# Kernel tuning notes

Measured on AMD Instinct MI355X. Metric: run time of the kernel, lower is better.

Reference implementation:

```python
import jax, jax.numpy as jnp
import numpy as np
from jax import lax

B, TENC, TMEL = 32, 512, 400
E, H, A, P, M, F, K = 512, 512, 512, 256, 128, 32, 31


def setup_inputs() -> dict:
    key = jax.random.key(0)
    ks = jax.random.split(key, 20)
    def rn(i, shape, fan_in):
        return jax.random.normal(ks[i], shape, jnp.float32) / np.float32(np.sqrt(fan_in))
    return dict(
        enc_outputs=jax.random.normal(ks[0], (B, TENC, 2 * E), jnp.float32),
        mel_spec_true=jax.random.normal(ks[1], (B, TMEL, M), jnp.float32),
        text_lens=jax.random.randint(ks[2], (B,), 0, TENC),
        mel_spec_lens=jax.random.randint(ks[3], (B,), 0, TMEL),
        max_text_len=TENC,
        pre_w1=rn(4, (M, P), M), pre_w2=rn(5, (P, P), P),
        attn_wi=rn(6, (P + E, 3 * H), P + E), attn_wh=rn(7, (H, 3 * H), H),
        attn_bi=jnp.zeros((3 * H,), jnp.float32), attn_bh=jnp.zeros((3 * H,), jnp.float32),
        q_w=rn(8, (H, A), H), k_w=rn(9, (2 * E, A), 2 * E),
        score_w=rn(10, (A, 1), A), score_b=jnp.zeros((1,), jnp.float32),
        loc_conv_w=rn(11, (F, 2, K), 2 * K), loc_w=rn(12, (F, A), F), loc_b=jnp.zeros((A,), jnp.float32),
        out_wi=rn(13, (A + H, 3 * H), A + H), out_wh=rn(14, (H, 3 * H), H),
        out_bi=jnp.zeros((3 * H,), jnp.float32), out_bh=jnp.zeros((3 * H,), jnp.float32),
        dec_w=rn(15, (H + A, M), H + A), dec_b=jnp.zeros((M,), jnp.float32),
        gate_w=rn(16, (H + A, 1), H + A), gate_b=jnp.zeros((1,), jnp.float32),
    )


def _gru_step(x, h, wi, wh, bi, bh):
    # single-step torch nn.GRU cell; gate order r, z, n
    gi = x @ wi + bi
    gh = h @ wh + bh
    ir, iz, inn = jnp.split(gi, 3, axis=-1)
    hr, hz, hn = jnp.split(gh, 3, axis=-1)
    r = jax.nn.sigmoid(ir + hr)
    z = jax.nn.sigmoid(iz + hz)
    n = jnp.tanh(inn + r * hn)
    return (1.0 - z) * n + z * h


def reference(enc_outputs, mel_spec_true, text_lens, mel_spec_lens, max_text_len,
              pre_w1, pre_w2, attn_wi, attn_wh, attn_bi, attn_bh,
              q_w, k_w, score_w, score_b, loc_conv_w, loc_w, loc_b,
              out_wi, out_wh, out_bi, out_bh, dec_w, dec_b, gate_w, gate_b):
    Bsz, Tenc, _ = enc_outputs.shape
    Tmel = mel_spec_true.shape[1]
    Hd = attn_wh.shape[0]
    Ad = k_w.shape[1]
    pad = (loc_conv_w.shape[2] - 1) // 2

    keys_p = enc_outputs @ k_w                                # [B,Tenc,A]
    enc_mask = jnp.arange(Tenc)[None, :] > text_lens[:, None]  # True = masked (t > len)

    def prenet(x):  # dropout disabled for determinism
        return jax.nn.relu(jax.nn.relu(x @ pre_w1) @ pre_w2)

    dec_in0 = prenet(jnp.zeros((Bsz, mel_spec_true.shape[2]), enc_outputs.dtype))
    carry0 = (jnp.zeros((Bsz, Hd), jnp.float32), jnp.zeros((Bsz, Hd), jnp.float32),
              jnp.zeros((Bsz, Tenc), jnp.float32), jnp.zeros((Bsz, Tenc), jnp.float32),
              jnp.zeros((Bsz, Ad), jnp.float32), dec_in0)

    def step(carry, _):
        h_attn, h_out, att_w, att_cum, ctx, dec_in = carry
        h_attn = _gru_step(jnp.concatenate([dec_in, ctx], -1), h_attn, attn_wi, attn_wh, attn_bi, attn_bh)
        loc_in = jnp.stack([att_w, att_cum], axis=1)           # [B,2,Tenc]
        loc = lax.conv_general_dilated(loc_in, loc_conv_w, (1,), [(pad, pad)],
                                       dimension_numbers=('NCH', 'OIH', 'NCH'))  # [B,F,Tenc]
        loc = jnp.swapaxes(loc, 1, 2) @ loc_w + loc_b          # [B,Tenc,A]
        q = (h_attn @ q_w)[:, None, :]                         # [B,1,A]
        s = (jnp.tanh(q + keys_p + loc) @ score_w + score_b)[..., 0]  # [B,Tenc]
        s = jnp.where(enc_mask, -jnp.inf, s)
        att_w = jax.nn.softmax(s, axis=1)
        ctx = jnp.einsum('bt,bta->ba', att_w, keys_p)
        att_cum = att_cum + att_w
        h_out = _gru_step(jnp.concatenate([h_attn, ctx], -1), h_out, out_wi, out_wh, out_bi, out_bh)
        att_h = jnp.concatenate([h_out, ctx], -1)
        mel = att_h @ dec_w + dec_b                            # [B,M]
        stop = (att_h @ gate_w + gate_b)[:, 0]                 # [B]
        dec_in = prenet(mel)                                   # teacher_force_ratio = 0
        return (h_attn, h_out, att_w, att_cum, ctx, dec_in), (mel, stop, att_w)

    _, (mels, gates, attns) = lax.scan(step, carry0, None, length=Tmel)
    mels = jnp.swapaxes(mels, 0, 1)    # [B,Tmel,M]
    gates = jnp.swapaxes(gates, 0, 1)  # [B,Tmel]
    attns = jnp.swapaxes(attns, 0, 1)  # [B,Tmel,Tenc]
    mel_mask = jnp.arange(Tmel)[None, :] > mel_spec_lens[:, None]
    masked_mel = jnp.where(mel_mask[:, :, None], 0.0, mels)
    masked_gate = jnp.where(mel_mask, 1000.0, gates)
    return masked_mel, masked_gate, attns, mel_mask
```

## Files before the change

kernel.cpp:

```cpp
#include <hip/hip_runtime.h>
#include <hip/hip_fp16.h>
#include <math.h>

#define NBLK 256
#define NTHR 1024

__device__ __forceinline__ float fast_rcp(float x) {
#if __has_builtin(__builtin_amdgcn_rcpf)
  return __builtin_amdgcn_rcpf(x);
#else
  return 1.f / x;
#endif
}
__device__ __forceinline__ float fast_sigmoid(float x) { return fast_rcp(1.f + __expf(-x)); }
__device__ __forceinline__ float fast_tanh(float x) { return 1.f - 2.f * fast_rcp(1.f + __expf(2.f * x)); }

union HU2 { unsigned int u; __half2 h; };
union HU4 { uint4 u; __half2 h[4]; };
__device__ __forceinline__ float2 cvt2(unsigned int u) { HU2 t; t.u = u; return __half22float2(t.h); }

__device__ __forceinline__ void sta(float* p, float v) {
  __hip_atomic_store(p, v, __ATOMIC_RELAXED, __HIP_MEMORY_SCOPE_AGENT);
}
__device__ __forceinline__ float lda(const float* p) {
  return __hip_atomic_load(p, __ATOMIC_RELAXED, __HIP_MEMORY_SCOPE_AGENT);
}
__device__ __forceinline__ int ldai(const int* p) {
  return __hip_atomic_load(p, __ATOMIC_RELAXED, __HIP_MEMORY_SCOPE_AGENT);
}
__device__ __forceinline__ void ntst(float* p, float v) { __builtin_nontemporal_store(v, p); }

struct Params {
  const float *enc, *pre_w1, *pre_w2, *attn_bi, *attn_bh;
  const float *q_w, *k_w, *score_w, *score_b, *conv_w, *loc_w, *loc_b;
  const float *out_bi, *out_bh, *dec_b, *gate_b;
  const float *attn_wi, *attn_wh, *out_wi, *out_wh, *dec_w, *gate_w;
  const int *text_lens, *mel_lens;
  __half *hkeys, *gw1T, *gw2T, *decT, *pre1T, *pre2T, *gateh, *locwh, *qwT;
  float *hA, *hO, *attw, *attcum, *decin, *ebuf, *zpart, *ctxacc, *ctxacc2, *stateZ;
  float *qbuf;
  int *done, *zdone, *done2, *hAdone, *qdone;
  float *out_mel, *out_gate, *out_attn, *out_mask;
};

__global__ __launch_bounds__(512) void k_keys(Params p) {
  __shared__ float sA[16][132];
  __shared__ float sB[16][68];
  int tid = threadIdx.x;
  int row0 = blockIdx.x * 128, col0 = blockIdx.y * 64;
  float acc[4][4] = {};
  int r = tid >> 2, kq = tid & 3;
  int tx = tid & 15, ty = tid >> 4;
  for (int k0 = 0; k0 < 1024; k0 += 16) {
    __syncthreads();
    float4 a4 = *(const float4*)(p.enc + (size_t)(row0 + r) * 1024 + k0 + kq * 4);
    sA[kq * 4 + 0][r] = a4.x; sA[kq * 4 + 1][r] = a4.y;
    sA[kq * 4 + 2][r] = a4.z; sA[kq * 4 + 3][r] = a4.w;
    if (tid < 256) {
      int kb = tid >> 4, nb = (tid & 15) * 4;
      float4 b4 = *(const float4*)(p.k_w + (size_t)(k0 + kb) * 512 + col0 + nb);
      sB[kb][nb + 0] = b4.x; sB[kb][nb + 1] = b4.y;
      sB[kb][nb + 2] = b4.z; sB[kb][nb + 3] = b4.w;
    }
    __syncthreads();
#pragma unroll
    for (int k = 0; k < 16; k++) {
      float ar[4], br[4];
#pragma unroll
      for (int i = 0; i < 4; i++) { ar[i] = sA[k][ty * 4 + i]; br[i] = sB[k][tx * 4 + i]; }
#pragma unroll
      for (int i = 0; i < 4; i++)
#pragma unroll
        for (int j = 0; j < 4; j++) acc[i][j] = fmaf(ar[i], br[j], acc[i][j]);
    }
  }
#pragma unroll
  for (int i = 0; i < 4; i++)
#pragma unroll
    for (int j = 0; j < 4; j++)
      p.hkeys[(size_t)(row0 + ty * 4 + i) * 512 + col0 + tx * 4 + j] = __float2half(acc[i][j]);
}

__global__ __launch_bounds__(256) void k_repack(Params p) {
  const int gsz = gridDim.x * 256;
  const int t0 = blockIdx.x * 256 + threadIdx.x;
  for (int i = t0; i < 1280 * 512; i += gsz) {
    int r = i >> 9, u = i & 511;
    const float* src = (r < 768) ? p.attn_wi + (size_t)r * 1536 : p.attn_wh + (size_t)(r - 768) * 1536;
    __half2* d = (__half2*)(p.gw1T + ((size_t)i << 2));
    d[0] = __halves2half2(__float2half(src[u]), __float2half(src[512 + u]));
    d[1] = __halves2half2(__float2half(src[1024 + u]), __float2half(0.f));
  }
  for (int i = t0; i < 1536 * 512; i += gsz) {
    int r = i >> 9, u = i & 511;
    const float* src = (r < 1024) ? p.out_wi + (size_t)r * 1536 : p.out_wh + (size_t)(r - 1024) * 1536;
    __half2* d = (__half2*)(p.gw2T + ((size_t)i << 2));
    d[0] = __halves2half2(__float2half(src[u]), __float2half(src[512 + u]));
    d[1] = __halves2half2(__float2half(src[1024 + u]), __float2half(0.f));
  }
  for (int i = t0; i < 512 * 512; i += gsz) {
    int k = i >> 9, a = i & 511;
    p.qwT[(size_t)a * 512 + k] = __float2half(p.q_w[(size_t)k * 512 + a]);
  }
  for (int i = t0; i < 1024 * 128; i += gsz) {
    int k = i >> 7, m = i & 127;
    p.decT[(size_t)m * 1024 + k] = __float2half(p.dec_w[(size_t)k * 128 + m]);
  }
  for (int i = t0; i < 1024; i += gsz) p.gateh[i] = __float2half(p.gate_w[i]);
  for (int i = t0; i < 16384; i += gsz) p.locwh[i] = __float2half(p.loc_w[i]);
  for (int i = t0; i < 128 * 256; i += gsz) {
    int m = i >> 8, pc = i & 255;
    p.pre1T[(size_t)pc * 128 + m] = __float2half(p.pre_w1[(size_t)m * 256 + pc]);
  }
  for (int i = t0; i < 256 * 256; i += gsz) {
    int k = i >> 8, pc = i & 255;
    p.pre2T[(size_t)pc * 256 + k] = __float2half(p.pre_w2[(size_t)k * 256 + pc]);
  }
  for (int i = t0; i < 106496; i += gsz) p.stateZ[i] = 0.f;
  for (int i = t0; i < 16384; i += gsz) p.ctxacc[i] = 0.f;
  for (int i = t0; i < 16384; i += gsz) p.ctxacc2[i] = 0.f;
  for (int i = t0; i < 512; i += gsz) p.qdone[i] = 0;
  for (int i = t0; i < 2048; i += gsz) p.zdone[i] = 0;
  for (int i = t0; i < 12800; i += gsz) {
    int b = i / 400, t = i - b * 400;
    p.out_mask[i] = (t > p.mel_lens[b]) ? 1.f : 0.f;
  }
}

struct SMemMega {
  __half keysL[64 * 512];
  float ctxL[4][520];
  float hA2[4][520];
  float hO2[4][520];
  float invZ[4];
  union {
    struct { float x[4][264]; float4 part4[16][64]; } gr;
    struct { float locS[64][33]; float aw[94]; float ac[94]; float hA_s[512];
             float qS[512]; float qp2[16][64]; float cpred[8][512]; float eS[64]; } s3;
    struct { float xh[1024]; float red[1024]; float mel[128]; float p1[256]; } s6;
  } u;
};

__device__ __forceinline__ void gchunk(const uint2* __restrict__ w,
                                       const float* __restrict__ x, int ks,
                                       int j0, int j1,
                                       float& a0, float& a1, float& a2) {
#pragma unroll 8
  for (int j = j0; j < j1; ++j) {
    uint2 wv = w[(size_t)j << 13];
    float xv = x[ks + (j << 4)];
    float2 f0 = cvt2(wv.x);
    float nf = cvt2(wv.y).x;
    a0 = fmaf(xv, f0.x, a0);
    a1 = fmaf(xv, f0.y, a1);
    a2 = fmaf(xv, nf, a2);
  }
}

__global__ __launch_bounds__(NTHR) void mega(Params p) {
  __shared__ SMemMega sm;
  const int blk = blockIdx.x, tid = threadIdx.x;
  const int ug = blk & 31, bg = blk >> 5, b0 = bg * 4;
  const int bS = blk & 31, t8 = blk >> 5, t0g = t8 << 6;

  const int u_ = tid & 15, b2_ = (tid >> 4) & 3, ks_ = tid >> 6;
  const int uG_ = (ug << 4) + u_;
  const uint2* w1 = (const uint2*)p.gw1T + ((size_t)ks_ << 9) + uG_;
  const uint2* w2 = (const uint2*)p.gw2T + ((size_t)ks_ << 9) + uG_;

  {
    const uint4* src = (const uint4*)(p.hkeys + (((size_t)(bS << 9) + t0g) << 9));
    uint4* dst = (uint4*)sm.keysL;
    for (int i = tid; i < 4096; i += NTHR) dst[i] = src[i];
    for (int i = tid; i < 2048; i += NTHR) sm.ctxL[i >> 9][i & 511] = 0.f;
  }
  __syncthreads();

  float g1r = 0.f, g1z = 0.f, g1ni = 0.f, g1nh = 0.f;

#pragma clang loop unroll(disable)
  for (int step = 0; step < 400; step++) {
    const int par = step & 1;
    float* hA_prev = p.hA + par * 16384;
    float* hA_next = p.hA + (par ^ 1) * 16384;
    float* hO_prev = p.hO + par * 16384;
    float* hO_next = p.hO + (par ^ 1) * 16384;
    float* cCur = par ? p.ctxacc2 : p.ctxacc;
    float* cNxt = par ? p.ctxacc : p.ctxacc2;

    float r2 = 0.f, z2 = 0.f, ni2 = 0.f, nh2 = 0.f;

    {
      if (step > 0) {
        if (tid < 4) {
          while (ldai(&p.done2[(b0 + tid) * 16]) < 4 * step)
            __builtin_amdgcn_s_sleep(2);
        }
        __syncthreads();
      }
      for (int i = tid; i < 1024; i += NTHR)
        sm.u.gr.x[i >> 8][i & 255] = lda(&p.decin[((b0 + (i >> 8)) << 8) + (i & 255)]);
      for (int i = tid; i < 2048; i += NTHR)
        sm.hO2[i >> 9][i & 511] = lda(&hO_prev[((b0 + (i >> 9)) << 9) + (i & 511)]);
      __syncthreads();
      gchunk(w1, &sm.u.gr.x[b2_][0], ks_, 0, 16, g1r, g1z, g1ni);
      sm.u.gr.part4[ks_][(u_ << 2) + b2_] = make_float4(g1r, g1z, g1ni, g1nh);
      __syncthreads();
      if (tid < 64) {
        int uu = tid >> 2, bb2 = tid & 3;
        float4 s = make_float4(0.f, 0.f, 0.f, 0.f);
#pragma unroll
        for (int l = 0; l < 16; l++) {
          float4 v = sm.u.gr.part4[l][(uu << 2) + bb2];
          s.x += v.x; s.y += v.y; s.z += v.z; s.w += v.w;
        }
        int uGf = (ug << 4) + uu;
        float r = fast_sigmoid(s.x + p.attn_bi[uGf] + p.attn_bh[uGf]);
        float z = fast_sigmoid(s.y + p.attn_bi[512 + uGf] + p.attn_bh[512 + uGf]);
        float n = fast_tanh(s.z + p.attn_bi[1024 + uGf] + r * (s.w + p.attn_bh[1024 + uGf]));
        float hv = lda(&hA_prev[((b0 + bb2) << 9) + uGf]);
        sta(&hA_next[((b0 + bb2) << 9) + uGf], (1.f - z) * n + z * hv);
      }
      asm volatile("s_waitcnt vmcnt(0)" ::: "memory");
      if (tid < 4) atomicAdd(&p.hAdone[(b0 + tid) * 16], 1);
      gchunk(w2, &sm.hO2[b2_][0] - 1024, ks_, 64, 96, r2, z2, nh2);
    }

    {
      for (int j = tid; j < 94; j += NTHR) {
        int pp = t0g - 15 + j;
        bool ok = (unsigned)pp < 512u;
        sm.u.s3.aw[j] = ok ? lda(&p.attw[(bS << 9) + pp]) : 0.f;
        sm.u.s3.ac[j] = ok ? lda(&p.attcum[(bS << 9) + pp]) : 0.f;
      }
      if (tid == 0) {
        while (ldai(&p.hAdone[bS * 16]) < 32 * (step + 1))
          __builtin_amdgcn_s_sleep(2);
      }
      __syncthreads();
      if (t8 == 0) {
        for (int i = tid; i < 512; i += NTHR) sta(&cNxt[(bS << 9) + i], 0.f);
      }
      if (tid < 512) sm.u.s3.hA_s[tid] = lda(&hA_next[(bS << 9) + tid]);
      __syncthreads();
      {
        int a = tid & 63, ks = tid >> 6;
        const HU4* qp = (const HU4*)(p.qwT + (size_t)(t0g + a) * 512 + ks * 32);
        float q0 = 0.f, q1 = 0.f;
#pragma unroll
        for (int it = 0; it < 4; it++) {
          HU4 raw = qp[it];
          int kb = ks * 32 + it * 8;
#pragma unroll
          for (int h2 = 0; h2 < 4; h2++) {
            float2 w = __half22float2(raw.h[h2]);
            q0 = fmaf(sm.u.s3.hA_s[kb + h2 * 2], w.x, q0);
            q1 = fmaf(sm.u.s3.hA_s[kb + h2 * 2 + 1], w.y, q1);
          }
        }
        sm.u.s3.qp2[ks][a] = q0 + q1;
      }
      __syncthreads();
      if (tid < 64) {
        float s = 0.f;
#pragma unroll
        for (int l = 0; l < 16; l++) s += sm.u.s3.qp2[l][tid];
        sta(&p.qbuf[(bS << 9) + t0g + tid], s + p.loc_b[t0g + tid]);
      }
      if (tid == 0) {
        asm volatile("s_waitcnt vmcnt(0)" ::: "memory");
        atomicAdd(&p.qdone[bS * 16], 1);
      }
      const int tlen = p.text_lens[bS];
      for (int i = tid; i < 2048; i += NTHR) {
        int tt = i >> 5, f = i & 31;
        const float* w0 = p.conv_w + f * 62;
        float a = 0.f;
#pragma unroll
        for (int k = 0; k < 31; k++)
          a = fmaf(w0[k], sm.u.s3.aw[tt + k], fmaf(w0[31 + k], sm.u.s3.ac[tt + k], a));
        sm.u.s3.locS[tt][f] = a;
      }
      if (tid == 0) {
        while (ldai(&p.qdone[bS * 16]) < 8 * (step + 1))
          __builtin_amdgcn_s_sleep(2);
      }
      __syncthreads();
      if (tid < 512) sm.u.s3.qS[tid] = lda(&p.qbuf[(bS << 9) + tid]);
      __syncthreads();
      const int lane = tid & 63, wv = tid >> 6;
      float acc[4][8];
      float4 qA = *(const float4*)&sm.u.s3.qS[lane * 8];
      float4 qB = *(const float4*)&sm.u.s3.qS[lane * 8 + 4];
#pragma unroll
      for (int j = 0; j < 4; j++) {
        int tL = wv * 4 + j;
        HU4 raw; raw.u = *(const uint4*)&sm.keysL[tL * 512 + lane * 8];
        float2 k0 = __half22float2(raw.h[0]), k1 = __half22float2(raw.h[1]);
        float2 k2 = __half22float2(raw.h[2]), k3 = __half22float2(raw.h[3]);
        acc[j][0] = qA.x + k0.x; acc[j][1] = qA.y + k0.y;
        acc[j][2] = qA.z + k1.x; acc[j][3] = qA.w + k1.y;
        acc[j][4] = qB.x + k2.x; acc[j][5] = qB.y + k2.y;
        acc[j][6] = qB.z + k3.x; acc[j][7] = qB.w + k3.y;
      }
#pragma unroll 4
      for (int f = 0; f < 32; f++) {
        HU4 rw; rw.u = *(const uint4*)(p.locwh + (size_t)f * 512 + lane * 8);
        float2 w0 = __half22float2(rw.h[0]), w1 = __half22float2(rw.h[1]);
        float2 w2v = __half22float2(rw.h[2]), w3 = __half22float2(rw.h[3]);
#pragma unroll
        for (int j = 0; j < 4; j++) {
          float lf = sm.u.s3.locS[wv * 4 + j][f];
          acc[j][0] = fmaf(lf, w0.x, acc[j][0]); acc[j][1] = fmaf(lf, w0.y, acc[j][1]);
          acc[j][2] = fmaf(lf, w1.x, acc[j][2]); acc[j][3] = fmaf(lf, w1.y, acc[j][3]);
          acc[j][4] = fmaf(lf, w2v.x, acc[j][4]); acc[j][5] = fmaf(lf, w2v.y, acc[j][5]);
          acc[j][6] = fmaf(lf, w3.x, acc[j][6]); acc[j][7] = fmaf(lf, w3.y, acc[j][7]);
        }
      }
      float4 sA = *(const float4*)(p.score_w + lane * 8);
      float4 sB = *(const float4*)(p.score_w + lane * 8 + 4);
      float sbias = p.score_b[0];
      float e_reg[4];
#pragma unroll
      for (int j = 0; j < 4; j++) {
        float pv = fast_tanh(acc[j][0]) * sA.x + fast_tanh(acc[j][1]) * sA.y +
                   fast_tanh(acc[j][2]) * sA.z + fast_tanh(acc[j][3]) * sA.w +
                   fast_tanh(acc[j][4]) * sB.x + fast_tanh(acc[j][5]) * sB.y +
                   fast_tanh(acc[j][6]) * sB.z + fast_tanh(acc[j][7]) * sB.w;
#pragma unroll
        for (int off = 32; off > 0; off >>= 1) pv += __shfl_xor(pv, off, 64);
        int t = t0g + wv * 4 + j;
        e_reg[j] = (t > tlen) ? 0.f : __expf(pv + sbias);
      }
      if (lane == 0) {
#pragma unroll
        for (int j = 0; j < 4; j++) sm.u.s3.eS[wv * 4 + j] = e_reg[j];
      }
      float cp[8] = {0.f, 0.f, 0.f, 0.f, 0.f, 0.f, 0.f, 0.f};
#pragma unroll
      for (int j = 0; j < 4; j++) {
        int tL = wv * 4 + j;
        HU4 raw; raw.u = *(const uint4*)&sm.keysL[tL * 512 + lane * 8];
        float2 k0 = __half22float2(raw.h[0]), k1 = __half22float2(raw.h[1]);
        float2 k2 = __half22float2(raw.h[2]), k3 = __half22float2(raw.h[3]);
        float e = e_reg[j];
        cp[0] = fmaf(e, k0.x, cp[0]); cp[1] = fmaf(e, k0.y, cp[1]);
        cp[2] = fmaf(e, k1.x, cp[2]); cp[3] = fmaf(e, k1.y, cp[3]);
        cp[4] = fmaf(e, k2.x, cp[4]); cp[5] = fmaf(e, k2.y, cp[5]);
        cp[6] = fmaf(e, k3.x, cp[6]); cp[7] = fmaf(e, k3.y, cp[7]);
      }
      __syncthreads();
      if (wv < 8) {
        float4* r0 = (float4*)&sm.u.s3.cpred[wv][lane * 8];
        r0[0] = make_float4(cp[0], cp[1], cp[2], cp[3]);
        r0[1] = make_float4(cp[4], cp[5], cp[6], cp[7]);
      }
      __syncthreads();
      if (wv >= 8) {
        float* r0 = &sm.u.s3.cpred[wv - 8][lane * 8];
#pragma unroll
        for (int i = 0; i < 8; i++) r0[i] += cp[i];
      }
      __syncthreads();
      if (tid < 512) {
        float s = 0.f;
#pragma unroll
        for (int j = 0; j < 8; j++) s += sm.u.s3.cpred[j][tid];
        atomicAdd(&cCur[(bS << 9) + tid], s);
      }
      if (tid < 64) {
        float e = sm.u.s3.eS[tid];
        sta(&p.ebuf[(bS << 9) + t0g + tid], e);
        float z = e;
#pragma unroll
        for (int off = 32; off > 0; off >>= 1) z += __shfl_xor(z, off, 64);
        if (tid == 0) sta(&p.zpart[bS * 8 + t8], z);
      }
      if (tid < 512 && (tid & 63) == 0) {
        asm volatile("s_waitcnt vmcnt(0)" ::: "memory");
        atomicAdd(&p.zdone[bS * 16], 1);
      }
      if (tid < 4) {
        while (ldai(&p.hAdone[(b0 + tid) * 16]) < 32 * (step + 1))
          __builtin_amdgcn_s_sleep(2);
      }
      __syncthreads();
      for (int i = tid; i < 2048; i += NTHR)
        sm.hA2[i >> 9][i & 511] = lda(&hA_next[((b0 + (i >> 9)) << 9) + (i & 511)]);
      __syncthreads();
      gchunk(w2, &sm.hA2[b2_][0], ks_, 0, 32, r2, z2, ni2);
    }

    {
      if (tid < 4) {
        while (ldai(&p.zdone[(b0 + tid) * 16]) < 64 * (step + 1))
          __builtin_amdgcn_s_sleep(2);
        float Z = 0.f;
#pragma unroll
        for (int j = 0; j < 8; j++) Z += lda(&p.zpart[(b0 + tid) * 8 + j]);
        sm.invZ[tid] = fast_rcp(Z);
      }
      __syncthreads();
      for (int i = tid; i < 2048; i += NTHR) {
        int b2 = i >> 9, a = i & 511;
        sm.ctxL[b2][a] = lda(&cCur[((b0 + b2) << 9) + a]) * sm.invZ[b2];
      }
      if (ug < 4) {
        const int bb = b0 + ug;
        if (tid < 512) {
          float v = lda(&p.ebuf[(bb << 9) + tid]) * sm.invZ[ug];
          sta(&p.attw[(bb << 9) + tid], v);
          float oc = lda(&p.attcum[(bb << 9) + tid]);
          sta(&p.attcum[(bb << 9) + tid], oc + v);
          ntst(&p.out_attn[(size_t)bb * 204800 + (size_t)step * 512 + tid], v);
        }
      }
      __syncthreads();
      gchunk(w2, &sm.ctxL[b2_][0] - 512, ks_, 32, 64, r2, z2, ni2);
      sm.u.gr.part4[ks_][(u_ << 2) + b2_] = make_float4(r2, z2, ni2, nh2);
      __syncthreads();
      if (tid < 64) {
        int uu = tid >> 2, bb2 = tid & 3;
        float4 s = make_float4(0.f, 0.f, 0.f, 0.f);
#pragma unroll
        for (int l = 0; l < 16; l++) {
          float4 v = sm.u.gr.part4[l][(uu << 2) + bb2];
          s.x += v.x; s.y += v.y; s.z += v.z; s.w += v.w;
        }
        int uGf = (ug << 4) + uu;
        float r = fast_sigmoid(s.x + p.out_bi[uGf] + p.out_bh[uGf]);
        float z = fast_sigmoid(s.y + p.out_bi[512 + uGf] + p.out_bh[512 + uGf]);
        float n = fast_tanh(s.z + p.out_bi[1024 + uGf] + r * (s.w + p.out_bh[1024 + uGf]));
        float hv = sm.hO2[bb2][uGf];
        sta(&hO_next[((b0 + bb2) << 9) + uGf], (1.f - z) * n + z * hv);
      }
      asm volatile("s_waitcnt vmcnt(0)" ::: "memory");
      if (tid < 4) atomicAdd(&p.done[(b0 + tid) * 16], 1);
      if (ug < 4) {
        const int bb = b0 + ug;
        if (tid == 0) {
          int target = 32 * (step + 1);
          while (ldai(&p.done[bb * 16]) < target)
            __builtin_amdgcn_s_sleep(2);
        }
        __syncthreads();
        sm.u.s6.xh[tid] = (tid < 512) ? lda(&hO_next[(bb << 9) + tid])
                                      : sm.ctxL[ug][tid - 512];
        __syncthreads();
        bool masked = step > p.mel_lens[bb];
        {
          int m = tid & 127, ks = tid >> 7;
          const HU4* dp = (const HU4*)(p.decT + (size_t)m * 1024 + ks * 128);
          float a = 0.f;
#pragma unroll 4
          for (int it = 0; it < 16; it++) {
            HU4 raw = dp[it];
            int kb = ks * 128 + it * 8;
#pragma unroll
            for (int h2 = 0; h2 < 4; h2++) {
              float2 w = __half22float2(raw.h[h2]);
              a = fmaf(sm.u.s6.xh[kb + h2 * 2], w.x, a);
              a = fmaf(sm.u.s6.xh[kb + h2 * 2 + 1], w.y, a);
            }
          }
          sm.u.s6.red[tid] = a;
        }
        __syncthreads();
        if (tid < 128) {
          float mv = p.dec_b[tid];
#pragma unroll
          for (int j = 0; j < 8; j++) mv += sm.u.s6.red[tid + j * 128];
          sm.u.s6.mel[tid] = mv;
          ntst(&p.out_mel[(size_t)bb * 51200 + (size_t)step * 128 + tid], masked ? 0.f : mv);
        }
        __syncthreads();
        sm.u.s6.red[tid] = sm.u.s6.xh[tid] * __half2float(p.gateh[tid]);
        __syncthreads();
        if (tid < 64) {
          float g = 0.f;
#pragma unroll
          for (int j = 0; j < 16; j++) g += sm.u.s6.red[tid + j * 64];
#pragma unroll
          for (int off = 32; off > 0; off >>= 1) g += __shfl_xor(g, off, 64);
          if (tid == 0) ntst(&p.out_gate[bb * 400 + step], masked ? 1000.f : (g + p.gate_b[0]));
        }
        __syncthreads();
        {
          int pc = tid & 255, ks = tid >> 8;
          const HU4* wp = (const HU4*)(p.pre1T + (size_t)pc * 128 + ks * 32);
          float a = 0.f;
#pragma unroll
          for (int it = 0; it < 4; it++) {
            HU4 raw = wp[it];
            int kb = ks * 32 + it * 8;
#pragma unroll
            for (int h2 = 0; h2 < 4; h2++) {
              float2 w = __half22float2(raw.h[h2]);
              a = fmaf(sm.u.s6.mel[kb + h2 * 2], w.x, a);
              a = fmaf(sm.u.s6.mel[kb + h2 * 2 + 1], w.y, a);
            }
          }
          sm.u.s6.red[tid] = a;
        }
        __syncthreads();
        if (tid < 256) {
          float a = sm.u.s6.red[tid] + sm.u.s6.red[tid + 256] +
                    sm.u.s6.red[tid + 512] + sm.u.s6.red[tid + 768];
          sm.u.s6.p1[tid] = fmaxf(a, 0.f);
        }
        __syncthreads();
        {
          int pc = tid & 255, ks = tid >> 8;
          const HU4* wp = (const HU4*)(p.pre2T + (size_t)pc * 256 + ks * 64);
          float a = 0.f;
#pragma unroll
          for (int it = 0; it < 8; it++) {
            HU4 raw = wp[it];
            int kb = ks * 64 + it * 8;
#pragma unroll
            for (int h2 = 0; h2 < 4; h2++) {
              float2 w = __half22float2(raw.h[h2]);
              a = fmaf(sm.u.s6.p1[kb + h2 * 2], w.x, a);
              a = fmaf(sm.u.s6.p1[kb + h2 * 2 + 1], w.y, a);
            }
          }
          sm.u.s6.red[tid] = a;
        }
        __syncthreads();
        if (tid < 256) {
          float a = sm.u.s6.red[tid] + sm.u.s6.red[tid + 256] +
                    sm.u.s6.red[tid + 512] + sm.u.s6.red[tid + 768];
          sta(&p.decin[(bb << 8) + tid], fmaxf(a, 0.f));
        }
        if (tid < 256 && (tid & 63) == 0) {
          asm volatile("s_waitcnt vmcnt(0)" ::: "memory");
          atomicAdd(&p.done2[bb * 16], 1);
        }
      }
      g1r = 0.f; g1z = 0.f; g1ni = 0.f; g1nh = 0.f;
      if (step < 399) {
        gchunk(w1, &sm.ctxL[b2_][0] - 256, ks_, 16, 48, g1r, g1z, g1ni);
        gchunk(w1, &sm.hA2[b2_][0] - 768, ks_, 48, 80, g1r, g1z, g1nh);
      }
    }
  }
}

extern "C" void kernel_launch(void* const* d_in, const int* in_sizes, int n_in,
                              void* d_out, int out_size, void* d_ws, size_t ws_size,
                              hipStream_t stream) {
  Params p;
  p.enc       = (const float*)d_in[0];
  p.text_lens = (const int*)d_in[2];
  p.mel_lens  = (const int*)d_in[3];
  p.pre_w1    = (const float*)d_in[5];
  p.pre_w2    = (const float*)d_in[6];
  p.attn_wi   = (const float*)d_in[7];
  p.attn_wh   = (const float*)d_in[8];
  p.attn_bi   = (const float*)d_in[9];
  p.attn_bh   = (const float*)d_in[10];
  p.q_w       = (const float*)d_in[11];
  p.k_w       = (const float*)d_in[12];
  p.score_w   = (const float*)d_in[13];
  p.score_b   = (const float*)d_in[14];
  p.conv_w    = (const float*)d_in[15];
  p.loc_w     = (const float*)d_in[16];
  p.loc_b     = (const float*)d_in[17];
  p.out_wi    = (const float*)d_in[18];
  p.out_wh    = (const float*)d_in[19];
  p.out_bi    = (const float*)d_in[20];
  p.out_bh    = (const float*)d_in[21];
  p.dec_w     = (const float*)d_in[22];
  p.dec_b     = (const float*)d_in[23];
  p.gate_w    = (const float*)d_in[24];
  p.gate_b    = (const float*)d_in[25];

  float* ws = (float*)d_ws;
  p.hkeys  = (__half*)(ws);
  p.gw1T   = (__half*)(ws + 4194304);
  p.gw2T   = (__half*)(ws + 5505024);
  p.decT   = (__half*)(ws + 7077888);
  p.pre1T  = (__half*)(ws + 7143424);
  p.pre2T  = (__half*)(ws + 7159808);
  p.gateh  = (__half*)(ws + 7192576);
  p.locwh  = (__half*)(ws + 7193088);
  p.qwT    = (__half*)(ws + 7201280);
  p.hA     = ws + 7332352;
  p.hO     = ws + 7365120;
  p.attw   = ws + 7397888;
  p.attcum = ws + 7414272;
  p.decin  = ws + 7430656;
  p.stateZ = p.hA;
  p.ebuf   = ws + 7438848;
  p.zpart  = ws + 7455232;
  p.ctxacc = ws + 7455488;
  p.qdone  = (int*)(ws + 7471904);
  p.ctxacc2 = ws + 7472416;
  p.zdone  = (int*)(ws + 7488800);
  p.done2  = (int*)(ws + 7489312);
  p.hAdone = (int*)(ws + 7489824);
  p.done   = (int*)(ws + 7490336);
  p.qbuf   = ws + 7490848;
  float* out = (float*)d_out;
  p.out_mel  = out;
  p.out_gate = out + 1638400;
  p.out_attn = out + 1651200;
  p.out_mask = out + 8204800;

  k_repack<<<2048, 256, 0, stream>>>(p);
  k_keys<<<dim3(128, 8), 512, 0, stream>>>(p);
  void* args[] = { (void*)&p };
  hipLaunchCooperativeKernel((const void*)mega, dim3(NBLK), dim3(NTHR), args, 0, stream);
}
```

Before: 37.60 ms.

## Distribute query and mel/gate projections across GRU blocks via partial sums

Each block that updates a 16-unit slice of the attention GRU now also computes a partial query projection from fp32 q_w and writes it to a partial buffer. Each block that updates a slice of the output GRU likewise computes partial mel and gate projections. Consumers then sum these partials, which removes the separate qbuf/qdone stage and the serial decoder matvec done by a few blocks. Completion counters now work per batch group with wave-granular increments, and a start-up barrier lets the partial buffers reuse the half-precision key workspace once every block has copied its keys into shared memory. The cost is more partial-sum traffic and fp32 weight reads in place of fp16 repacked weights.

Measured after the change: 53.33 ms. 41.8% more time.

```diff
diff --git a/kernel.cpp b/kernel.cpp
--- a/kernel.cpp
+++ b/kernel.cpp
@@ -36,10 +36,10 @@
   const float *out_bi, *out_bh, *dec_b, *gate_b;
   const float *attn_wi, *attn_wh, *out_wi, *out_wh, *dec_w, *gate_w;
   const int *text_lens, *mel_lens;
-  __half *hkeys, *gw1T, *gw2T, *decT, *pre1T, *pre2T, *gateh, *locwh, *qwT;
+  __half *hkeys, *gw1T, *gw2T, *pre1T, *pre2T, *locwh;
   float *hA, *hO, *attw, *attcum, *decin, *ebuf, *zpart, *ctxacc, *ctxacc2, *stateZ;
-  float *qbuf;
-  int *done, *zdone, *done2, *hAdone, *qdone;
+  float *qpart, *melpart, *gatepart;
+  int *done, *zdone, *done2, *hAdone, *initbar;
   float *out_mel, *out_gate, *out_attn, *out_mask;
 };
 
@@ -98,15 +98,6 @@
     d[0] = __halves2half2(__float2half(src[u]), __float2half(src[512 + u]));
     d[1] = __halves2half2(__float2half(src[1024 + u]), __float2half(0.f));
   }
-  for (int i = t0; i < 512 * 512; i += gsz) {
-    int k = i >> 9, a = i & 511;
-    p.qwT[(size_t)a * 512 + k] = __float2half(p.q_w[(size_t)k * 512 + a]);
-  }
-  for (int i = t0; i < 1024 * 128; i += gsz) {
-    int k = i >> 7, m = i & 127;
-    p.decT[(size_t)m * 1024 + k] = __float2half(p.dec_w[(size_t)k * 128 + m]);
-  }
-  for (int i = t0; i < 1024; i += gsz) p.gateh[i] = __float2half(p.gate_w[i]);
   for (int i = t0; i < 16384; i += gsz) p.locwh[i] = __float2half(p.loc_w[i]);
   for (int i = t0; i < 128 * 256; i += gsz) {
     int m = i >> 8, pc = i & 255;
@@ -119,7 +110,6 @@
   for (int i = t0; i < 106496; i += gsz) p.stateZ[i] = 0.f;
   for (int i = t0; i < 16384; i += gsz) p.ctxacc[i] = 0.f;
   for (int i = t0; i < 16384; i += gsz) p.ctxacc2[i] = 0.f;
-  for (int i = t0; i < 512; i += gsz) p.qdone[i] = 0;
   for (int i = t0; i < 2048; i += gsz) p.zdone[i] = 0;
   for (int i = t0; i < 12800; i += gsz) {
     int b = i / 400, t = i - b * 400;
@@ -134,10 +124,11 @@
   float hO2[4][520];
   float invZ[4];
   union {
-    struct { float x[4][264]; float4 part4[16][64]; } gr;
-    struct { float locS[64][33]; float aw[94]; float ac[94]; float hA_s[512];
-             float qS[512]; float qp2[16][64]; float cpred[8][512]; float eS[64]; } s3;
-    struct { float xh[1024]; float red[1024]; float mel[128]; float p1[256]; } s6;
+    struct { float x[4][264]; float4 part4[16][64];
+             float hAslice[4][16]; float hOslice[4][16]; } gr;
+    struct { float locS[64][33]; float aw[94]; float ac[94];
+             float qS[512]; float cpred[8][512]; float eS[64]; } s3;
+    struct { float red[1024]; float mel[132]; float p1[264]; } s6;
   } u;
 };
 
@@ -162,6 +153,7 @@
   const int blk = blockIdx.x, tid = threadIdx.x;
   const int ug = blk & 31, bg = blk >> 5, b0 = bg * 4;
   const int bS = blk & 31, t8 = blk >> 5, t0g = t8 << 6;
+  const int bgS = bS >> 2;
 
   const int u_ = tid & 15, b2_ = (tid >> 4) & 3, ks_ = tid >> 6;
   const int uG_ = (ug << 4) + u_;
@@ -172,7 +164,16 @@
     const uint4* src = (const uint4*)(p.hkeys + (((size_t)(bS << 9) + t0g) << 9));
     uint4* dst = (uint4*)sm.keysL;
     for (int i = tid; i < 4096; i += NTHR) dst[i] = src[i];
-    for (int i = tid; i < 2048; i += NTHR) sm.ctxL[i >> 9][i & 511] = 0.f;
+    for (int i = tid; i < 2048; i += NTHR) {
+      sm.ctxL[i >> 9][i & 511] = 0.f;
+      sm.hA2[i >> 9][i & 511] = 0.f;
+      sm.hO2[i >> 9][i & 511] = 0.f;
+    }
+  }
+  __syncthreads();
+  if (tid == 0) {
+    atomicAdd(p.initbar, 1);
+    while (ldai(p.initbar) < NBLK) __builtin_amdgcn_s_sleep(2);
   }
   __syncthreads();
 
@@ -192,8 +193,8 @@
 
     {
       if (step > 0) {
-        if (tid < 4) {
-          while (ldai(&p.done2[(b0 + tid) * 16]) < 4 * step)
+        if (tid == 0) {
+          while (ldai(&p.done2[bg * 16]) < 16 * step)
             __builtin_amdgcn_s_sleep(2);
         }
         __syncthreads();
@@ -219,58 +220,44 @@
         float z = fast_sigmoid(s.y + p.attn_bi[512 + uGf] + p.attn_bh[512 + uGf]);
         float n = fast_tanh(s.z + p.attn_bi[1024 + uGf] + r * (s.w + p.attn_bh[1024 + uGf]));
         float hv = lda(&hA_prev[((b0 + bb2) << 9) + uGf]);
-        sta(&hA_next[((b0 + bb2) << 9) + uGf], (1.f - z) * n + z * hv);
-      }
-      asm volatile("s_waitcnt vmcnt(0)" ::: "memory");
-      if (tid < 4) atomicAdd(&p.hAdone[(b0 + tid) * 16], 1);
+        float hnew = (1.f - z) * n + z * hv;
+        sta(&hA_next[((b0 + bb2) << 9) + uGf], hnew);
+        sm.u.gr.hAslice[bb2][uu] = hnew;
+      }
+      __syncthreads();
+      {
+        int a = tid & 511, bh = tid >> 9;
+        const float* qw = p.q_w + ((size_t)(ug << 4)) * 512 + a;
+        float s0 = 0.f, s1 = 0.f;
+#pragma unroll
+        for (int u = 0; u < 16; u++) {
+          float w = qw[(size_t)u * 512];
+          s0 = fmaf(sm.u.gr.hAslice[bh * 2][u], w, s0);
+          s1 = fmaf(sm.u.gr.hAslice[bh * 2 + 1][u], w, s1);
+        }
+        int base = ((((b0 + bh * 2) << 5) | ug) << 9) + a;
+        sta(&p.qpart[base], s0);
+        sta(&p.qpart[base + (1 << 14)], s1);
+      }
+      if ((tid & 63) == 0) {
+        asm volatile("s_waitcnt vmcnt(0)" ::: "memory");
+        atomicAdd(&p.hAdone[bg * 16], 1);
+      }
       gchunk(w2, &sm.hO2[b2_][0] - 1024, ks_, 64, 96, r2, z2, nh2);
     }
 
     {
+      __syncthreads();
       for (int j = tid; j < 94; j += NTHR) {
         int pp = t0g - 15 + j;
         bool ok = (unsigned)pp < 512u;
         sm.u.s3.aw[j] = ok ? lda(&p.attw[(bS << 9) + pp]) : 0.f;
         sm.u.s3.ac[j] = ok ? lda(&p.attcum[(bS << 9) + pp]) : 0.f;
       }
-      if (tid == 0) {
-        while (ldai(&p.hAdone[bS * 16]) < 32 * (step + 1))
-          __builtin_amdgcn_s_sleep(2);
-      }
-      __syncthreads();
       if (t8 == 0) {
         for (int i = tid; i < 512; i += NTHR) sta(&cNxt[(bS << 9) + i], 0.f);
       }
-      if (tid < 512) sm.u.s3.hA_s[tid] = lda(&hA_next[(bS << 9) + tid]);
-      __syncthreads();
-      {
-        int a = tid & 63, ks = tid >> 6;
-        const HU4* qp = (const HU4*)(p.qwT + (size_t)(t0g + a) * 512 + ks * 32);
-        float q0 = 0.f, q1 = 0.f;
-#pragma unroll
-        for (int it = 0; it < 4; it++) {
-          HU4 raw = qp[it];
-          int kb = ks * 32 + it * 8;
-#pragma unroll
-          for (int h2 = 0; h2 < 4; h2++) {
-            float2 w = __half22float2(raw.h[h2]);
-            q0 = fmaf(sm.u.s3.hA_s[kb + h2 * 2], w.x, q0);
-            q1 = fmaf(sm.u.s3.hA_s[kb + h2 * 2 + 1], w.y, q1);
-          }
-        }
-        sm.u.s3.qp2[ks][a] = q0 + q1;
-      }
-      __syncthreads();
-      if (tid < 64) {
-        float s = 0.f;
-#pragma unroll
-        for (int l = 0; l < 16; l++) s += sm.u.s3.qp2[l][tid];
-        sta(&p.qbuf[(bS << 9) + t0g + tid], s + p.loc_b[t0g + tid]);
-      }
-      if (tid == 0) {
-        asm volatile("s_waitcnt vmcnt(0)" ::: "memory");
-        atomicAdd(&p.qdone[bS * 16], 1);
-      }
+      __syncthreads();
       const int tlen = p.text_lens[bS];
       for (int i = tid; i < 2048; i += NTHR) {
         int tt = i >> 5, f = i & 31;
@@ -282,11 +269,21 @@
         sm.u.s3.locS[tt][f] = a;
       }
       if (tid == 0) {
-        while (ldai(&p.qdone[bS * 16]) < 8 * (step + 1))
+        while (ldai(&p.hAdone[bgS * 16]) < 512 * (step + 1))
           __builtin_amdgcn_s_sleep(2);
       }
       __syncthreads();
-      if (tid < 512) sm.u.s3.qS[tid] = lda(&p.qbuf[(bS << 9) + tid]);
+      {
+        int a = tid & 511, h = tid >> 9;
+        const float* qp = p.qpart + (((size_t)(bS << 5) + (h << 4)) << 9) + a;
+        float s = 0.f;
+#pragma unroll
+        for (int g = 0; g < 16; g++) s += lda(qp + ((size_t)g << 9));
+        sm.u.s3.cpred[h][a] = s;
+      }
+      __syncthreads();
+      if (tid < 512)
+        sm.u.s3.qS[tid] = sm.u.s3.cpred[0][tid] + sm.u.s3.cpred[1][tid] + p.loc_b[tid];
       __syncthreads();
       const int lane = tid & 63, wv = tid >> 6;
       float acc[4][8];
@@ -378,10 +375,10 @@
       }
       if (tid < 512 && (tid & 63) == 0) {
         asm volatile("s_waitcnt vmcnt(0)" ::: "memory");
-        atomicAdd(&p.zdone[bS * 16], 1);
-      }
-      if (tid < 4) {
-        while (ldai(&p.hAdone[(b0 + tid) * 16]) < 32 * (step + 1))
+        atomicAdd(&p.zdone[bgS * 16], 1);
+      }
+      if (tid == 0) {
+        while (ldai(&p.hAdone[bg * 16]) < 512 * (step + 1))
           __builtin_amdgcn_s_sleep(2);
       }
       __syncthreads();
@@ -392,9 +389,12 @@
     }
 
     {
+      if (tid == 0) {
+        while (ldai(&p.zdone[bg * 16]) < 256 * (step + 1))
+          __builtin_amdgcn_s_sleep(2);
+      }
+      __syncthreads();
       if (tid < 4) {
-        while (ldai(&p.zdone[(b0 + tid) * 16]) < 64 * (step + 1))
-          __builtin_amdgcn_s_sleep(2);
         float Z = 0.f;
 #pragma unroll
         for (int j = 0; j < 8; j++) Z += lda(&p.zpart[(b0 + tid) * 8 + j]);
@@ -405,15 +405,13 @@
         int b2 = i >> 9, a = i & 511;
         sm.ctxL[b2][a] = lda(&cCur[((b0 + b2) << 9) + a]) * sm.invZ[b2];
       }
-      if (ug < 4) {
+      if (ug < 4 && tid < 512) {
         const int bb = b0 + ug;
-        if (tid < 512) {
-          float v = lda(&p.ebuf[(bb << 9) + tid]) * sm.invZ[ug];
-          sta(&p.attw[(bb << 9) + tid], v);
-          float oc = lda(&p.attcum[(bb << 9) + tid]);
-          sta(&p.attcum[(bb << 9) + tid], oc + v);
-          ntst(&p.out_attn[(size_t)bb * 204800 + (size_t)step * 512 + tid], v);
-        }
+        float v = lda(&p.ebuf[(bb << 9) + tid]) * sm.invZ[ug];
+        sta(&p.attw[(bb << 9) + tid], v);
+        float oc = lda(&p.attcum[(bb << 9) + tid]);
+        sta(&p.attcum[(bb << 9) + tid], oc + v);
+        ntst(&p.out_attn[(size_t)bb * 204800 + (size_t)step * 512 + tid], v);
       }
       __syncthreads();
       gchunk(w2, &sm.ctxL[b2_][0] - 512, ks_, 32, 64, r2, z2, ni2);
@@ -432,57 +430,65 @@
         float z = fast_sigmoid(s.y + p.out_bi[512 + uGf] + p.out_bh[512 + uGf]);
         float n = fast_tanh(s.z + p.out_bi[1024 + uGf] + r * (s.w + p.out_bh[1024 + uGf]));
         float hv = sm.hO2[bb2][uGf];
-        sta(&hO_next[((b0 + bb2) << 9) + uGf], (1.f - z) * n + z * hv);
-      }
-      asm volatile("s_waitcnt vmcnt(0)" ::: "memory");
-      if (tid < 4) atomicAdd(&p.done[(b0 + tid) * 16], 1);
+        float hnew = (1.f - z) * n + z * hv;
+        sta(&hO_next[((b0 + bb2) << 9) + uGf], hnew);
+        sm.u.gr.hOslice[bb2][uu] = hnew;
+      }
+      __syncthreads();
+      if (tid < 512) {
+        int b = tid >> 7, m = tid & 127;
+        const float* dw = p.dec_w + ((size_t)(ug << 4)) * 128 + m;
+        const float* dw2 = p.dec_w + ((size_t)(512 + (ug << 4))) * 128 + m;
+        float a = 0.f;
+#pragma unroll
+        for (int u = 0; u < 16; u++) {
+          a = fmaf(sm.u.gr.hOslice[b][u], dw[(size_t)u * 128], a);
+          a = fmaf(sm.ctxL[b][(ug << 4) + u], dw2[(size_t)u * 128], a);
+        }
+        sta(&p.melpart[((((b0 + b) << 5) | ug) << 7) + m], a);
+        if (m == 0) {
+          const float* gw = p.gate_w + (ug << 4);
+          float g = 0.f;
+#pragma unroll
+          for (int u = 0; u < 16; u++) {
+            g = fmaf(sm.u.gr.hOslice[b][u], gw[u], g);
+            g = fmaf(sm.ctxL[b][(ug << 4) + u], gw[512 + u], g);
+          }
+          sta(&p.gatepart[((b0 + b) << 5) | ug], g);
+        }
+      }
+      if ((tid & 63) == 0) {
+        asm volatile("s_waitcnt vmcnt(0)" ::: "memory");
+        atomicAdd(&p.done[bg * 16], 1);
+      }
+      g1r = 0.f; g1z = 0.f; g1ni = 0.f; g1nh = 0.f;
+      if (step < 399) {
+        gchunk(w1, &sm.ctxL[b2_][0] - 256, ks_, 16, 48, g1r, g1z, g1ni);
+        gchunk(w1, &sm.hA2[b2_][0] - 768, ks_, 48, 80, g1r, g1z, g1nh);
+      }
       if (ug < 4) {
         const int bb = b0 + ug;
         if (tid == 0) {
-          int target = 32 * (step + 1);
-          while (ldai(&p.done[bb * 16]) < target)
+          while (ldai(&p.done[bg * 16]) < 512 * (step + 1))
             __builtin_amdgcn_s_sleep(2);
         }
-        __syncthreads();
-        sm.u.s6.xh[tid] = (tid < 512) ? lda(&hO_next[(bb << 9) + tid])
-                                      : sm.ctxL[ug][tid - 512];
         __syncthreads();
         bool masked = step > p.mel_lens[bb];
-        {
-          int m = tid & 127, ks = tid >> 7;
-          const HU4* dp = (const HU4*)(p.decT + (size_t)m * 1024 + ks * 128);
-          float a = 0.f;
-#pragma unroll 4
-          for (int it = 0; it < 16; it++) {
-            HU4 raw = dp[it];
-            int kb = ks * 128 + it * 8;
-#pragma unroll
-            for (int h2 = 0; h2 < 4; h2++) {
-              float2 w = __half22float2(raw.h[h2]);
-              a = fmaf(sm.u.s6.xh[kb + h2 * 2], w.x, a);
-              a = fmaf(sm.u.s6.xh[kb + h2 * 2 + 1], w.y, a);
-            }
-          }
-          sm.u.s6.red[tid] = a;
-        }
-        __syncthreads();
         if (tid < 128) {
+          const float* mp = p.melpart + (((size_t)(bb << 5)) << 7) + tid;
           float mv = p.dec_b[tid];
 #pragma unroll
-          for (int j = 0; j < 8; j++) mv += sm.u.s6.red[tid + j * 128];
+          for (int g = 0; g < 32; g++) mv += lda(mp + (g << 7));
           sm.u.s6.mel[tid] = mv;
           ntst(&p.out_mel[(size_t)bb * 51200 + (size_t)step * 128 + tid], masked ? 0.f : mv);
         }
-        __syncthreads();
-        sm.u.s6.red[tid] = sm.u.s6.xh[tid] * __half2float(p.gateh[tid]);
-        __syncthreads();
-        if (tid < 64) {
-          float g = 0.f;
-#pragma unroll
-          for (int j = 0; j < 16; j++) g += sm.u.s6.red[tid + j * 64];
-#pragma unroll
-          for (int off = 32; off > 0; off >>= 1) g += __shfl_xor(g, off, 64);
-          if (tid == 0) ntst(&p.out_gate[bb * 400 + step], masked ? 1000.f : (g + p.gate_b[0]));
+        if (tid >= 128 && tid < 192) {
+          int l = tid & 63;
+          float g = (l < 32) ? lda(&p.gatepart[(bb << 5) + l]) : 0.f;
+#pragma unroll
+          for (int off = 16; off > 0; off >>= 1) g += __shfl_xor(g, off, 64);
+          if (l == 0)
+            ntst(&p.out_gate[bb * 400 + step], masked ? 1000.f : (g + p.gate_b[0]));
         }
         __syncthreads();
         {
@@ -534,13 +540,8 @@
         }
         if (tid < 256 && (tid & 63) == 0) {
           asm volatile("s_waitcnt vmcnt(0)" ::: "memory");
-          atomicAdd(&p.done2[bb * 16], 1);
-        }
-      }
-      g1r = 0.f; g1z = 0.f; g1ni = 0.f; g1nh = 0.f;
-      if (step < 399) {
-        gchunk(w1, &sm.ctxL[b2_][0] - 256, ks_, 16, 48, g1r, g1z, g1ni);
-        gchunk(w1, &sm.hA2[b2_][0] - 768, ks_, 48, 80, g1r, g1z, g1nh);
+          atomicAdd(&p.done2[bg * 16], 1);
+        }
       }
     }
   }
@@ -577,14 +578,14 @@
 
   float* ws = (float*)d_ws;
   p.hkeys  = (__half*)(ws);
+  p.qpart  = ws;
+  p.melpart = ws + 524288;
+  p.gatepart = ws + 655360;
   p.gw1T   = (__half*)(ws + 4194304);
   p.gw2T   = (__half*)(ws + 5505024);
-  p.decT   = (__half*)(ws + 7077888);
   p.pre1T  = (__half*)(ws + 7143424);
   p.pre2T  = (__half*)(ws + 7159808);
-  p.gateh  = (__half*)(ws + 7192576);
   p.locwh  = (__half*)(ws + 7193088);
-  p.qwT    = (__half*)(ws + 7201280);
   p.hA     = ws + 7332352;
   p.hO     = ws + 7365120;
   p.attw   = ws + 7397888;
@@ -594,13 +595,13 @@
   p.ebuf   = ws + 7438848;
   p.zpart  = ws + 7455232;
   p.ctxacc = ws + 7455488;
-  p.qdone  = (int*)(ws + 7471904);
   p.ctxacc2 = ws + 7472416;
-  p.zdone  = (int*)(ws + 7488800);
-  p.done2  = (int*)(ws + 7489312);
-  p.hAdone = (int*)(ws + 7489824);
-  p.done   = (int*)(ws + 7490336);
-  p.qbuf   = ws + 7490848;
+  int* fb  = (int*)(ws + 7488800);
+  p.zdone  = fb;
+  p.done2  = fb + 128;
+  p.hAdone = fb + 256;
+  p.done   = fb + 384;
+  p.initbar = fb + 1920;
   float* out = (float*)d_out;
   p.out_mel  = out;
   p.out_gate = out + 1638400;
```

## Coarsen sync flags to batch groups and hoist location conv before waits

Applied to the files above, without the earlier changes.

Per-batch completion counters become per-batch-group counters, so one thread polls a single flag instead of four threads polling four. The location convolution and the location-weight projection now run before waiting on the hA and q flags, overlapping that work with the producer latency. The next step's input-GRU partial products are issued right after the hO update, before the decoder wait, instead of at the end of the step. The flag buffers are relaid out into one contiguous region with a new zeroing pass, adding some risk around counter targets and initialization.

New measurement: 37.33 ms. About the same (-0.7%).

```diff
diff --git a/kernel.cpp b/kernel.cpp
--- a/kernel.cpp
+++ b/kernel.cpp
@@ -119,8 +119,7 @@
   for (int i = t0; i < 106496; i += gsz) p.stateZ[i] = 0.f;
   for (int i = t0; i < 16384; i += gsz) p.ctxacc[i] = 0.f;
   for (int i = t0; i < 16384; i += gsz) p.ctxacc2[i] = 0.f;
-  for (int i = t0; i < 512; i += gsz) p.qdone[i] = 0;
-  for (int i = t0; i < 2048; i += gsz) p.zdone[i] = 0;
+  for (int i = t0; i < 2048; i += gsz) p.hAdone[i] = 0;
   for (int i = t0; i < 12800; i += gsz) {
     int b = i / 400, t = i - b * 400;
     p.out_mask[i] = (t > p.mel_lens[b]) ? 1.f : 0.f;
@@ -162,6 +161,7 @@
   const int blk = blockIdx.x, tid = threadIdx.x;
   const int ug = blk & 31, bg = blk >> 5, b0 = bg * 4;
   const int bS = blk & 31, t8 = blk >> 5, t0g = t8 << 6;
+  const int bgS = bS >> 2;
 
   const int u_ = tid & 15, b2_ = (tid >> 4) & 3, ks_ = tid >> 6;
   const int uG_ = (ug << 4) + u_;
@@ -172,7 +172,11 @@
     const uint4* src = (const uint4*)(p.hkeys + (((size_t)(bS << 9) + t0g) << 9));
     uint4* dst = (uint4*)sm.keysL;
     for (int i = tid; i < 4096; i += NTHR) dst[i] = src[i];
-    for (int i = tid; i < 2048; i += NTHR) sm.ctxL[i >> 9][i & 511] = 0.f;
+    for (int i = tid; i < 2048; i += NTHR) {
+      sm.ctxL[i >> 9][i & 511] = 0.f;
+      sm.hA2[i >> 9][i & 511] = 0.f;
+      sm.hO2[i >> 9][i & 511] = 0.f;
+    }
   }
   __syncthreads();
 
@@ -192,8 +196,8 @@
 
     {
       if (step > 0) {
-        if (tid < 4) {
-          while (ldai(&p.done2[(b0 + tid) * 16]) < 4 * step)
+        if (tid == 0) {
+          while (ldai(&p.done2[bg * 16]) < 16 * step)
             __builtin_amdgcn_s_sleep(2);
         }
         __syncthreads();
@@ -222,25 +226,37 @@
         sta(&hA_next[((b0 + bb2) << 9) + uGf], (1.f - z) * n + z * hv);
       }
       asm volatile("s_waitcnt vmcnt(0)" ::: "memory");
-      if (tid < 4) atomicAdd(&p.hAdone[(b0 + tid) * 16], 1);
+      if (tid == 0) atomicAdd(&p.hAdone[bg * 16], 1);
       gchunk(w2, &sm.hO2[b2_][0] - 1024, ks_, 64, 96, r2, z2, nh2);
     }
 
     {
+      __syncthreads();
       for (int j = tid; j < 94; j += NTHR) {
         int pp = t0g - 15 + j;
         bool ok = (unsigned)pp < 512u;
         sm.u.s3.aw[j] = ok ? lda(&p.attw[(bS << 9) + pp]) : 0.f;
         sm.u.s3.ac[j] = ok ? lda(&p.attcum[(bS << 9) + pp]) : 0.f;
       }
-      if (tid == 0) {
-        while (ldai(&p.hAdone[bS * 16]) < 32 * (step + 1))
-          __builtin_amdgcn_s_sleep(2);
-      }
-      __syncthreads();
       if (t8 == 0) {
         for (int i = tid; i < 512; i += NTHR) sta(&cNxt[(bS << 9) + i], 0.f);
       }
+      __syncthreads();
+      const int tlen = p.text_lens[bS];
+      for (int i = tid; i < 2048; i += NTHR) {
+        int tt = i >> 5, f = i & 31;
+        const float* w0 = p.conv_w + f * 62;
+        float a = 0.f;
+#pragma unroll
+        for (int k = 0; k < 31; k++)
+          a = fmaf(w0[k], sm.u.s3.aw[tt + k], fmaf(w0[31 + k], sm.u.s3.ac[tt + k], a));
+        sm.u.s3.locS[tt][f] = a;
+      }
+      if (tid == 0) {
+        while (ldai(&p.hAdone[bgS * 16]) < 32 * (step + 1))
+          __builtin_amdgcn_s_sleep(2);
+      }
+      __syncthreads();
       if (tid < 512) sm.u.s3.hA_s[tid] = lda(&hA_next[(bS << 9) + tid]);
       __syncthreads();
       {
@@ -271,38 +287,8 @@
         asm volatile("s_waitcnt vmcnt(0)" ::: "memory");
         atomicAdd(&p.qdone[bS * 16], 1);
       }
-      const int tlen = p.text_lens[bS];
-      for (int i = tid; i < 2048; i += NTHR) {
-        int tt = i >> 5, f = i & 31;
-        const float* w0 = p.conv_w + f * 62;
-        float a = 0.f;
-#pragma unroll
-        for (int k = 0; k < 31; k++)
-          a = fmaf(w0[k], sm.u.s3.aw[tt + k], fmaf(w0[31 + k], sm.u.s3.ac[tt + k], a));
-        sm.u.s3.locS[tt][f] = a;
-      }
-      if (tid == 0) {
-        while (ldai(&p.qdone[bS * 16]) < 8 * (step + 1))
-          __builtin_amdgcn_s_sleep(2);
-      }
-      __syncthreads();
-      if (tid < 512) sm.u.s3.qS[tid] = lda(&p.qbuf[(bS << 9) + tid]);
-      __syncthreads();
       const int lane = tid & 63, wv = tid >> 6;
-      float acc[4][8];
-      float4 qA = *(const float4*)&sm.u.s3.qS[lane * 8];
-      float4 qB = *(const float4*)&sm.u.s3.qS[lane * 8 + 4];
-#pragma unroll
-      for (int j = 0; j < 4; j++) {
-        int tL = wv * 4 + j;
-        HU4 raw; raw.u = *(const uint4*)&sm.keysL[tL * 512 + lane * 8];
-        float2 k0 = __half22float2(raw.h[0]), k1 = __half22float2(raw.h[1]);
-        float2 k2 = __half22float2(raw.h[2]), k3 = __half22float2(raw.h[3]);
-        acc[j][0] = qA.x + k0.x; acc[j][1] = qA.y + k0.y;
-        acc[j][2] = qA.z + k1.x; acc[j][3] = qA.w + k1.y;
-        acc[j][4] = qB.x + k2.x; acc[j][5] = qB.y + k2.y;
-        acc[j][6] = qB.z + k3.x; acc[j][7] = qB.w + k3.y;
-      }
+      float acc[4][8] = {};
 #pragma unroll 4
       for (int f = 0; f < 32; f++) {
         HU4 rw; rw.u = *(const uint4*)(p.locwh + (size_t)f * 512 + lane * 8);
@@ -316,6 +302,26 @@
           acc[j][4] = fmaf(lf, w2v.x, acc[j][4]); acc[j][5] = fmaf(lf, w2v.y, acc[j][5]);
           acc[j][6] = fmaf(lf, w3.x, acc[j][6]); acc[j][7] = fmaf(lf, w3.y, acc[j][7]);
         }
+      }
+      if (tid == 0) {
+        while (ldai(&p.qdone[bS * 16]) < 8 * (step + 1))
+          __builtin_amdgcn_s_sleep(2);
+      }
+      __syncthreads();
+      if (tid < 512) sm.u.s3.qS[tid] = lda(&p.qbuf[(bS << 9) + tid]);
+      __syncthreads();
+      float4 qA = *(const float4*)&sm.u.s3.qS[lane * 8];
+      float4 qB = *(const float4*)&sm.u.s3.qS[lane * 8 + 4];
+#pragma unroll
+      for (int j = 0; j < 4; j++) {
+        int tL = wv * 4 + j;
+        HU4 raw; raw.u = *(const uint4*)&sm.keysL[tL * 512 + lane * 8];
+        float2 k0 = __half22float2(raw.h[0]), k1 = __half22float2(raw.h[1]);
+        float2 k2 = __half22float2(raw.h[2]), k3 = __half22float2(raw.h[3]);
+        acc[j][0] += qA.x + k0.x; acc[j][1] += qA.y + k0.y;
+        acc[j][2] += qA.z + k1.x; acc[j][3] += qA.w + k1.y;
+        acc[j][4] += qB.x + k2.x; acc[j][5] += qB.y + k2.y;
+        acc[j][6] += qB.z + k3.x; acc[j][7] += qB.w + k3.y;
       }
       float4 sA = *(const float4*)(p.score_w + lane * 8);
       float4 sB = *(const float4*)(p.score_w + lane * 8 + 4);
@@ -378,10 +384,10 @@
       }
       if (tid < 512 && (tid & 63) == 0) {
         asm volatile("s_waitcnt vmcnt(0)" ::: "memory");
-        atomicAdd(&p.zdone[bS * 16], 1);
-      }
-      if (tid < 4) {
-        while (ldai(&p.hAdone[(b0 + tid) * 16]) < 32 * (step + 1))
+        atomicAdd(&p.zdone[bgS * 16], 1);
+      }
+      if (tid == 0) {
+        while (ldai(&p.hAdone[bg * 16]) < 32 * (step + 1))
           __builtin_amdgcn_s_sleep(2);
       }
       __syncthreads();
@@ -392,9 +398,12 @@
     }
 
     {
+      if (tid == 0) {
+        while (ldai(&p.zdone[bg * 16]) < 256 * (step + 1))
+          __builtin_amdgcn_s_sleep(2);
+      }
+      __syncthreads();
       if (tid < 4) {
-        while (ldai(&p.zdone[(b0 + tid) * 16]) < 64 * (step + 1))
-          __builtin_amdgcn_s_sleep(2);
         float Z = 0.f;
 #pragma unroll
         for (int j = 0; j < 8; j++) Z += lda(&p.zpart[(b0 + tid) * 8 + j]);
@@ -405,15 +414,13 @@
         int b2 = i >> 9, a = i & 511;
         sm.ctxL[b2][a] = lda(&cCur[((b0 + b2) << 9) + a]) * sm.invZ[b2];
       }
-      if (ug < 4) {
+      if (ug < 4 && tid < 512) {
         const int bb = b0 + ug;
-        if (tid < 512) {
-          float v = lda(&p.ebuf[(bb << 9) + tid]) * sm.invZ[ug];
-          sta(&p.attw[(bb << 9) + tid], v);
-          float oc = lda(&p.attcum[(bb << 9) + tid]);
-          sta(&p.attcum[(bb << 9) + tid], oc + v);
-          ntst(&p.out_attn[(size_t)bb * 204800 + (size_t)step * 512 + tid], v);
-        }
+        float v = lda(&p.ebuf[(bb << 9) + tid]) * sm.invZ[ug];
+        sta(&p.attw[(bb << 9) + tid], v);
+        float oc = lda(&p.attcum[(bb << 9) + tid]);
+        sta(&p.attcum[(bb << 9) + tid], oc + v);
+        ntst(&p.out_attn[(size_t)bb * 204800 + (size_t)step * 512 + tid], v);
       }
       __syncthreads();
       gchunk(w2, &sm.ctxL[b2_][0] - 512, ks_, 32, 64, r2, z2, ni2);
@@ -435,12 +442,16 @@
         sta(&hO_next[((b0 + bb2) << 9) + uGf], (1.f - z) * n + z * hv);
       }
       asm volatile("s_waitcnt vmcnt(0)" ::: "memory");
-      if (tid < 4) atomicAdd(&p.done[(b0 + tid) * 16], 1);
+      if (tid == 0) atomicAdd(&p.done[bg * 16], 1);
+      g1r = 0.f; g1z = 0.f; g1ni = 0.f; g1nh = 0.f;
+      if (step < 399) {
+        gchunk(w1, &sm.ctxL[b2_][0] - 256, ks_, 16, 48, g1r, g1z, g1ni);
+        gchunk(w1, &sm.hA2[b2_][0] - 768, ks_, 48, 80, g1r, g1z, g1nh);
+      }
       if (ug < 4) {
         const int bb = b0 + ug;
         if (tid == 0) {
-          int target = 32 * (step + 1);
-          while (ldai(&p.done[bb * 16]) < target)
+          while (ldai(&p.done[bg * 16]) < 32 * (step + 1))
             __builtin_amdgcn_s_sleep(2);
         }
         __syncthreads();
@@ -534,13 +545,8 @@
         }
         if (tid < 256 && (tid & 63) == 0) {
           asm volatile("s_waitcnt vmcnt(0)" ::: "memory");
-          atomicAdd(&p.done2[bb * 16], 1);
-        }
-      }
-      g1r = 0.f; g1z = 0.f; g1ni = 0.f; g1nh = 0.f;
-      if (step < 399) {
-        gchunk(w1, &sm.ctxL[b2_][0] - 256, ks_, 16, 48, g1r, g1z, g1ni);
-        gchunk(w1, &sm.hA2[b2_][0] - 768, ks_, 48, 80, g1r, g1z, g1nh);
+          atomicAdd(&p.done2[bg * 16], 1);
+        }
       }
     }
   }
@@ -594,12 +600,13 @@
   p.ebuf   = ws + 7438848;
   p.zpart  = ws + 7455232;
   p.ctxacc = ws + 7455488;
-  p.qdone  = (int*)(ws + 7471904);
   p.ctxacc2 = ws + 7472416;
-  p.zdone  = (int*)(ws + 7488800);
-  p.done2  = (int*)(ws + 7489312);
-  p.hAdone = (int*)(ws + 7489824);
-  p.done   = (int*)(ws + 7490336);
+  int* fb  = (int*)(ws + 7488800);
+  p.hAdone = fb;
+  p.zdone  = fb + 128;
+  p.done   = fb + 256;
+  p.done2  = fb + 384;
+  p.qdone  = fb + 512;
   p.qbuf   = ws + 7490848;
   float* out = (float*)d_out;
   p.out_mel  = out;
```
